# Kernel tuning notes

Measured on AMD Instinct MI355X. Metric: run time of the kernel, lower is better.

The kernel has to match this reference:

```python
import jax, jax.numpy as jnp
import numpy as np

LN_EPS = 1e-5   # torch nn.LayerNorm default
EPS = 1e-6      # module eps for denominator clamp


def _layernorm(x, gamma, beta):
    mu = jnp.mean(x, axis=-1, keepdims=True)
    var = jnp.mean(jnp.square(x - mu), axis=-1, keepdims=True)
    return (x - mu) * jax.lax.rsqrt(var + LN_EPS) * gamma + beta


def _l2norm(x):
    # torch F.normalize(dim=-1): x / max(||x||_2, 1e-12)
    n = jnp.sqrt(jnp.sum(jnp.square(x), axis=-1, keepdims=True))
    return x / jnp.maximum(n, 1e-12)


def setup_inputs() -> dict:
    key = jax.random.key(0)
    kq, kk, kv, kp = jax.random.split(key, 4)
    B, H, T, D = 4, 8, 8192, 64
    num_features = 256
    q = jax.random.normal(kq, (B, H, T, D), dtype=jnp.float32)
    k = jax.random.normal(kk, (B, H, T, D), dtype=jnp.float32)
    v = jax.random.normal(kv, (B, H, T, D), dtype=jnp.float32)
    # _create_projection with ortho=True: QR of (D, num_features) reduced -> Q is (D, D)
    g = jax.random.normal(kp, (D, num_features), dtype=jnp.float32)
    Q, _ = jnp.linalg.qr(g, mode='reduced')            # (D, D) since num_features > D
    proj = Q / jnp.maximum(jnp.sqrt(jnp.sum(Q * Q, axis=0, keepdims=True)), 1e-12)
    proj = proj * (D ** -0.25)
    gamma = jnp.ones((D,), dtype=jnp.float32)
    beta = jnp.zeros((D,), dtype=jnp.float32)
    return {"q": q, "k": k, "v": v, "proj": proj, "gamma": gamma, "beta": beta}


def reference(q, k, v, proj, gamma, beta):
    # LayerNorm over head_dim applied to q, k, v (the torch reshapes are a no-op
    # on the math: it is a per-(b,h,t) LayerNorm over the last dim D)
    qn = _layernorm(q, gamma, beta)
    kn = _layernorm(k, gamma, beta)
    vn = _layernorm(v, gamma, beta)
    qn = _l2norm(qn)
    kn = _l2norm(kn)
    # exp feature maps (clamped), scaled by 0.1
    q_proj = jnp.exp(jnp.clip(jnp.einsum('bhtn,nm->bhtm', qn, proj), -15.0, 15.0)) * 0.1
    k_proj = jnp.exp(jnp.clip(jnp.einsum('bhtn,nm->bhtm', kn, proj), -15.0, 15.0)) * 0.1
    # linear-attention accumulation
    kv = jnp.einsum('bhtm,bhtn->bhmn', k_proj, vn) * 0.1          # [B,H,M,D]
    qkv = jnp.einsum('bhtm,bhmn->bhtn', q_proj, kv) * 0.1         # [B,H,T,D]
    denom = jnp.sum(q_proj * k_proj, axis=-1, keepdims=True)      # [B,H,T,1]
    denom = jnp.maximum(denom, EPS)
    out = qkv / denom
    out = _layernorm(out, gamma, beta)                             # final LN over D
    return out  # [B,H,T,D]
```

## Files before the change

### kernel.cpp

```cpp
#include <hip/hip_runtime.h>
#include <stdint.h>
#include <stddef.h>

#define T_    8192
#define D_    64
#define BH_   32
#define CH_   32
#define ROWS_ (T_/CH_)
#define ITERS_ (ROWS_/64)
#define TS    72
#define LN_EPS 1e-5f
#define EPS_   1e-6f

#define PART_SZ   ((size_t)CH_*BH_*D_*D_*4)
#define KVF_OFF   (PART_SZ)
#define KVF_SZ    ((size_t)BH_*D_*D_*4)
#define WS_NEED   (KVF_OFF+KVF_SZ)

typedef __attribute__((ext_vector_type(8))) short bh8;
typedef __attribute__((ext_vector_type(4))) short bh4;
typedef __attribute__((ext_vector_type(4))) float f32x4;

__device__ __forceinline__ float bf2f(unsigned short u){ return __uint_as_float(((unsigned)u)<<16); }
__device__ __forceinline__ unsigned short f2bf(float f){
  unsigned u = __float_as_uint(f);
  return (unsigned short)((u + 0x7fffu + ((u>>16)&1u)) >> 16);
}
__device__ __forceinline__ void unp8(uint4 a, float* x){
  x[0]=__uint_as_float(a.x<<16); x[1]=__uint_as_float(a.x&0xffff0000u);
  x[2]=__uint_as_float(a.y<<16); x[3]=__uint_as_float(a.y&0xffff0000u);
  x[4]=__uint_as_float(a.z<<16); x[5]=__uint_as_float(a.z&0xffff0000u);
  x[6]=__uint_as_float(a.w<<16); x[7]=__uint_as_float(a.w&0xffff0000u);
}
__device__ __forceinline__ uint4 pk8(const float* x){
  uint4 r;
  r.x = (unsigned)f2bf(x[0]) | ((unsigned)f2bf(x[1])<<16);
  r.y = (unsigned)f2bf(x[2]) | ((unsigned)f2bf(x[3])<<16);
  r.z = (unsigned)f2bf(x[4]) | ((unsigned)f2bf(x[5])<<16);
  r.w = (unsigned)f2bf(x[6]) | ((unsigned)f2bf(x[7])<<16);
  return r;
}
__device__ __forceinline__ bool is_bf16_buf(const void* gamma){
  return ((const uint32_t*)gamma)[0] != 0x3F800000u;
}
__device__ __forceinline__ int vswb(int d){ return (((d&7) ^ ((d>>3)&6)) << 3); }

template<bool BF>
__device__ __forceinline__ float ldf(const void* p, long long i){
  if (BF) return bf2f(((const unsigned short*)p)[i]);
  else    return ((const float*)p)[i];
}
template<bool BF>
__device__ __forceinline__ void ld8f(const void* p, long long i, float* x){
  if (BF){ uint4 a = *(const uint4*)((const unsigned short*)p + i); unp8(a,x); }
  else {
    const float* f=(const float*)p + i;
    float4 a=*(const float4*)f, b=*(const float4*)(f+4);
    x[0]=a.x;x[1]=a.y;x[2]=a.z;x[3]=a.w; x[4]=b.x;x[5]=b.y;x[6]=b.z;x[7]=b.w;
  }
}
template<bool BF>
__device__ __forceinline__ void ld16f(const void* p, long long i, float* x){
  ld8f<BF>(p, i, x); ld8f<BF>(p, i+8, x+8);
}

__device__ __forceinline__ void ln16(float* x, const float* __restrict__ smg,
                                     const float* __restrict__ smb, int c, bool l2){
  float s=0.f;
  #pragma unroll
  for(int j=0;j<16;++j) s+=x[j];
  s += __shfl_xor(s,1); s += __shfl_xor(s,2);
  const float mu = s*(1.f/64.f);
  float vs=0.f;
  #pragma unroll
  for(int j=0;j<16;++j){ x[j]-=mu; vs=fmaf(x[j],x[j],vs); }
  vs += __shfl_xor(vs,1); vs += __shfl_xor(vs,2);
  const float rs = rsqrtf(vs*(1.f/64.f)+LN_EPS);
  float ss=0.f;
  #pragma unroll
  for(int j4=0;j4<4;++j4){
    const float4 g4 = *(const float4*)&smg[c*16+j4*4];
    const float4 b4 = *(const float4*)&smb[c*16+j4*4];
    float* xp = x + 4*j4;
    xp[0]=fmaf(xp[0]*rs, g4.x, b4.x); ss=fmaf(xp[0],xp[0],ss);
    xp[1]=fmaf(xp[1]*rs, g4.y, b4.y); ss=fmaf(xp[1],xp[1],ss);
    xp[2]=fmaf(xp[2]*rs, g4.z, b4.z); ss=fmaf(xp[2],xp[2],ss);
    xp[3]=fmaf(xp[3]*rs, g4.w, b4.w); ss=fmaf(xp[3],xp[3],ss);
  }
  if(l2){
    ss += __shfl_xor(ss,1); ss += __shfl_xor(ss,2);
    const float inv = rsqrtf(fmaxf(ss,1e-24f));
    #pragma unroll
    for(int j=0;j<16;++j) x[j]*=inv;
  }
}

template<bool BF, bool PART>
__device__ __forceinline__ void kv_body(const void* __restrict__ kg, const void* __restrict__ vg,
               const void* __restrict__ projg, const void* __restrict__ gammag,
               const void* __restrict__ betag, float* __restrict__ kvout,
               short* sm_a, short* sm_vt, short* sm_kt, float* smgb){
  const int tid=threadIdx.x, lane=tid&63, w=tid>>6;
  const int q4=lane>>4, l16=lane&15;
  const int r=lane>>2,  c=lane&3;
  const int bh=blockIdx.x;
  const long long base=(long long)bh*T_*D_;
  const int t0b=blockIdx.y*ROWS_;
  const float* smg = smgb;
  const float* smb = smgb+64;

  if (tid < 128){
    const int j = tid & 63;
    smgb[tid] = (tid<64) ? ldf<BF>(gammag,j) : ldf<BF>(betag,j);
  }
  for(int e=tid*8; e<D_*D_; e+=256*8){
    int d=e>>6, m=e&63;
    float t8[8]; ld8f<BF>(projg, e, t8);
    *(uint4*)&sm_a[d*TS+m] = pk8(t8);
  }
  __syncthreads();
  bh8 bP[4][2];
  #pragma unroll
  for(int nt=0;nt<4;++nt)
    #pragma unroll
    for(int ks=0;ks<2;++ks)
      #pragma unroll
      for(int j=0;j<8;++j)
        bP[nt][ks][j] = sm_a[(ks*32+q4*8+j)*TS + nt*16+l16];
  __syncthreads();

  f32x4 acc2[4];
  #pragma unroll
  for(int nt=0;nt<4;++nt) acc2[nt]=(f32x4){0.f,0.f,0.f,0.f};

  for(int it=0; it<ITERS_; ++it){
    const int tl=16*w;
    const long long gro = base + (long long)(t0b + it*64 + tl + r)*D_ + c*16;

    float xk[16], xv[16];
    ld16f<BF>(kg, gro, xk);
    ld16f<BF>(vg, gro, xv);

    ln16(xk, smg, smb, c, true);
    *(uint4*)&sm_a[(tl+r)*TS + c*16    ] = pk8(xk);
    *(uint4*)&sm_a[(tl+r)*TS + c*16 + 8] = pk8(xk+8);

    ln16(xv, smg, smb, c, false);
    #pragma unroll
    for(int j=0;j<16;++j){
      const int d=c*16+j;
      sm_vt[d*TS + ((tl+r) ^ vswb(d))] = (short)f2bf(xv[j]);
    }

    f32x4 c1[4];
    #pragma unroll
    for(int nt=0;nt<4;++nt) c1[nt]=(f32x4){0.f,0.f,0.f,0.f};
    #pragma unroll
    for(int ks=0;ks<2;++ks){
      bh8 af = *(const bh8*)&sm_a[(tl+l16)*TS + ks*32 + q4*8];
      #pragma unroll
      for(int nt=0;nt<4;++nt)
        c1[nt] = __builtin_amdgcn_mfma_f32_16x16x32_bf16(af, bP[nt][ks], c1[nt], 0,0,0);
    }
    #pragma unroll
    for(int nt=0;nt<4;++nt){
      bh4 p;
      #pragma unroll
      for(int reg=0;reg<4;++reg){
        float e = 0.1f*__expf(fminf(fmaxf(c1[nt][reg],-15.f),15.f));
        p[reg] = (short)f2bf(e);
      }
      *(bh4*)&sm_kt[(nt*16+l16)*TS + tl + q4*4] = p;
    }
    __syncthreads();

    #pragma unroll
    for(int ks=0;ks<2;++ks){
      bh8 af = *(const bh8*)&sm_kt[(tl+l16)*TS + ks*32 + q4*8];
      #pragma unroll
      for(int nt=0;nt<4;++nt){
        const int dn = nt*16+l16;
        bh8 bv = *(const bh8*)&sm_vt[dn*TS + ((ks*32+q4*8) ^ vswb(dn))];
        acc2[nt] = __builtin_amdgcn_mfma_f32_16x16x32_bf16(af, bv, acc2[nt], 0,0,0);
      }
    }
    __syncthreads();
  }

  if (PART){
    float* dst = kvout + ((size_t)blockIdx.y*BH_ + bh)*D_*D_;
    #pragma unroll
    for(int nt=0;nt<4;++nt)
      #pragma unroll
      for(int reg=0;reg<4;++reg)
        dst[(16*w + q4*4 + reg)*D_ + nt*16 + l16] = acc2[nt][reg]*0.1f;
  } else {
    float* dst = kvout + bh*D_*D_;
    #pragma unroll
    for(int nt=0;nt<4;++nt)
      #pragma unroll
      for(int reg=0;reg<4;++reg)
        atomicAdd(&dst[(16*w + q4*4 + reg)*D_ + nt*16 + l16], acc2[nt][reg]*0.1f);
  }
}

__global__ __launch_bounds__(256,4)
void reduce_kernel(const float* __restrict__ part, float* __restrict__ kvf){
  const int idx = blockIdx.x*256 + threadIdx.x;
  float s = 0.f;
  #pragma unroll 8
  for(int ch=0; ch<CH_; ++ch) s += part[(size_t)ch*BH_*D_*D_ + idx];
  kvf[idx] = s;
}

template<bool BF>
__device__ __forceinline__ void attn_body(const void* __restrict__ qg, const void* __restrict__ kg,
                 const void* __restrict__ projg, const void* __restrict__ gammag,
                 const void* __restrict__ betag, const float* __restrict__ kvg,
                 void* __restrict__ outg,
                 short* sm_qn, short* sm_kn, short* sm_qp, short* sm_kvT, float* smgb){
  const int tid=threadIdx.x, lane=tid&63, w=tid>>6;
  const int q4=lane>>4, l16=lane&15;
  const int r=lane>>2,  c=lane&3;
  const int bh=blockIdx.x;
  const long long base=(long long)bh*T_*D_;
  const int t0b=blockIdx.y*ROWS_;
  const float* smg = smgb;
  const float* smb = smgb+64;

  if (tid < 128){
    const int j = tid & 63;
    smgb[tid] = (tid<64) ? ldf<BF>(gammag,j) : ldf<BF>(betag,j);
  }
  for(int e=tid*8; e<D_*D_; e+=256*8){
    int d=e>>6, m=e&63;
    float t8[8]; ld8f<BF>(projg, e, t8);
    *(uint4*)&sm_qn[d*TS+m] = pk8(t8);
  }
  {
    const float* kvsrc = kvg + bh*D_*D_;
    for(int e=tid; e<D_*D_; e+=256){
      int f=e>>6, d=e&63;
      sm_kvT[d*TS + (f ^ vswb(d))] = (short)f2bf(kvsrc[e]);
    }
  }
  __syncthreads();
  bh8 bP[4][2];
  #pragma unroll
  for(int nt=0;nt<4;++nt)
    #pragma unroll
    for(int ks=0;ks<2;++ks)
      #pragma unroll
      for(int j=0;j<8;++j)
        bP[nt][ks][j] = sm_qn[(ks*32+q4*8+j)*TS + nt*16+l16];
  __syncthreads();

  for(int it=0; it<ITERS_; ++it){
    const int tl=16*w;
    const long long gro = base + (long long)(t0b + it*64 + tl + r)*D_ + c*16;

    float x[16];
    ld16f<BF>(qg, gro, x);
    ln16(x, smg, smb, c, true);
    *(uint4*)&sm_qn[(tl+r)*TS + c*16    ] = pk8(x);
    *(uint4*)&sm_qn[(tl+r)*TS + c*16 + 8] = pk8(x+8);
    ld16f<BF>(kg, gro, x);
    ln16(x, smg, smb, c, true);
    *(uint4*)&sm_kn[(tl+r)*TS + c*16    ] = pk8(x);
    *(uint4*)&sm_kn[(tl+r)*TS + c*16 + 8] = pk8(x+8);

    f32x4 qp[4], kp[4];
    #pragma unroll
    for(int nt=0;nt<4;++nt) qp[nt]=(f32x4){0.f,0.f,0.f,0.f};
    #pragma unroll
    for(int ks=0;ks<2;++ks){
      bh8 af = *(const bh8*)&sm_qn[(tl+l16)*TS + ks*32 + q4*8];
      #pragma unroll
      for(int nt=0;nt<4;++nt)
        qp[nt] = __builtin_amdgcn_mfma_f32_16x16x32_bf16(af, bP[nt][ks], qp[nt], 0,0,0);
    }
    #pragma unroll
    for(int nt=0;nt<4;++nt)
      #pragma unroll
      for(int reg=0;reg<4;++reg){
        float e = 0.1f*__expf(fminf(fmaxf(qp[nt][reg],-15.f),15.f));
        qp[nt][reg] = e;
        sm_qp[(tl+q4*4+reg)*TS + nt*16+l16] = (short)f2bf(e);
      }

    #pragma unroll
    for(int nt=0;nt<4;++nt) kp[nt]=(f32x4){0.f,0.f,0.f,0.f};
    #pragma unroll
    for(int ks=0;ks<2;++ks){
      bh8 af = *(const bh8*)&sm_kn[(tl+l16)*TS + ks*32 + q4*8];
      #pragma unroll
      for(int nt=0;nt<4;++nt)
        kp[nt] = __builtin_amdgcn_mfma_f32_16x16x32_bf16(af, bP[nt][ks], kp[nt], 0,0,0);
    }
    float sc[4];
    #pragma unroll
    for(int reg=0;reg<4;++reg){
      float dd=0.f;
      #pragma unroll
      for(int nt=0;nt<4;++nt){
        float kv = 0.1f*__expf(fminf(fmaxf(kp[nt][reg],-15.f),15.f));
        dd = fmaf(qp[nt][reg], kv, dd);
      }
      dd += __shfl_xor(dd,1); dd += __shfl_xor(dd,2);
      dd += __shfl_xor(dd,4); dd += __shfl_xor(dd,8);
      sc[reg] = 0.1f / fmaxf(dd, EPS_);
    }

    f32x4 c3[4];
    #pragma unroll
    for(int nt=0;nt<4;++nt) c3[nt]=(f32x4){0.f,0.f,0.f,0.f};
    #pragma unroll
    for(int ks=0;ks<2;++ks){
      bh8 af = *(const bh8*)&sm_qp[(tl+l16)*TS + ks*32 + q4*8];
      #pragma unroll
      for(int nt=0;nt<4;++nt){
        const int dn = nt*16+l16;
        bh8 bf = *(const bh8*)&sm_kvT[dn*TS + ((ks*32+q4*8) ^ vswb(dn))];
        c3[nt] = __builtin_amdgcn_mfma_f32_16x16x32_bf16(af, bf, c3[nt], 0,0,0);
      }
    }

    float rs4[4];
    #pragma unroll
    for(int reg=0;reg<4;++reg){
      float s=0.f;
      #pragma unroll
      for(int nt=0;nt<4;++nt){ c3[nt][reg] *= sc[reg]; s += c3[nt][reg]; }
      s += __shfl_xor(s,1); s += __shfl_xor(s,2); s += __shfl_xor(s,4); s += __shfl_xor(s,8);
      const float mu = s*(1.f/64.f);
      float vs=0.f;
      #pragma unroll
      for(int nt=0;nt<4;++nt){ const float dd=c3[nt][reg]-mu; c3[nt][reg]=dd; vs=fmaf(dd,dd,vs); }
      vs += __shfl_xor(vs,1); vs += __shfl_xor(vs,2); vs += __shfl_xor(vs,4); vs += __shfl_xor(vs,8);
      rs4[reg] = rsqrtf(vs*(1.f/64.f)+LN_EPS);
    }
    const long long obase = base + (long long)(t0b + it*64 + tl + q4*4)*D_ + l16;
    #pragma unroll
    for(int reg=0;reg<4;++reg)
      #pragma unroll
      for(int nt=0;nt<4;++nt){
        const float z = fmaf(c3[nt][reg]*rs4[reg], smg[nt*16+l16], smb[nt*16+l16]);
        const long long oi = obase + (long long)reg*D_ + nt*16;
        if (BF) ((unsigned short*)outg)[oi] = f2bf(z);
        else    ((float*)outg)[oi]          = z;
      }
  }
}

__global__ __launch_bounds__(256,4)
void kv_kernel_part(const void* __restrict__ kg, const void* __restrict__ vg,
                    const void* __restrict__ projg, const void* __restrict__ gammag,
                    const void* __restrict__ betag, float* __restrict__ part){
  __shared__ __align__(16) short sm_a [64*TS];
  __shared__ __align__(16) short sm_vt[64*TS];
  __shared__ __align__(16) short sm_kt[64*TS];
  __shared__ __align__(16) float smgb[128];
  if (is_bf16_buf(gammag)) kv_body<true ,true>(kg,vg,projg,gammag,betag,part,sm_a,sm_vt,sm_kt,smgb);
  else                     kv_body<false,true>(kg,vg,projg,gammag,betag,part,sm_a,sm_vt,sm_kt,smgb);
}

__global__ __launch_bounds__(256,4)
void kv_kernel_atomic(const void* __restrict__ kg, const void* __restrict__ vg,
                      const void* __restrict__ projg, const void* __restrict__ gammag,
                      const void* __restrict__ betag, float* __restrict__ kvg){
  __shared__ __align__(16) short sm_a [64*TS];
  __shared__ __align__(16) short sm_vt[64*TS];
  __shared__ __align__(16) short sm_kt[64*TS];
  __shared__ __align__(16) float smgb[128];
  if (is_bf16_buf(gammag)) kv_body<true ,false>(kg,vg,projg,gammag,betag,kvg,sm_a,sm_vt,sm_kt,smgb);
  else                     kv_body<false,false>(kg,vg,projg,gammag,betag,kvg,sm_a,sm_vt,sm_kt,smgb);
}

__global__ __launch_bounds__(256,4)
void attn_kernel(const void* __restrict__ qg, const void* __restrict__ kg,
                 const void* __restrict__ projg, const void* __restrict__ gammag,
                 const void* __restrict__ betag, const float* __restrict__ kvg,
                 void* __restrict__ outg){
  __shared__ __align__(16) short sm_qn [64*TS];
  __shared__ __align__(16) short sm_kn [64*TS];
  __shared__ __align__(16) short sm_qp [64*TS];
  __shared__ __align__(16) short sm_kvT[64*TS];
  __shared__ __align__(16) float smgb[128];
  if (is_bf16_buf(gammag)) attn_body<true >(qg,kg,projg,gammag,betag,kvg,outg,sm_qn,sm_kn,sm_qp,sm_kvT,smgb);
  else                     attn_body<false>(qg,kg,projg,gammag,betag,kvg,outg,sm_qn,sm_kn,sm_qp,sm_kvT,smgb);
}

extern "C" void kernel_launch(void* const* d_in, const int* in_sizes, int n_in,
                              void* d_out, int out_size, void* d_ws, size_t ws_size,
                              hipStream_t stream){
  const void* q     = d_in[0];
  const void* k     = d_in[1];
  const void* v     = d_in[2];
  const void* proj  = d_in[3];
  const void* gamma = d_in[4];
  const void* beta  = d_in[5];

  dim3 g(BH_, CH_);
  if (ws_size >= WS_NEED){
    float* part = (float*)d_ws;
    float* kvf  = (float*)((char*)d_ws + KVF_OFF);
    kv_kernel_part<<<g, 256, 0, stream>>>(k, v, proj, gamma, beta, part);
    reduce_kernel<<<dim3(BH_*D_*D_/256), 256, 0, stream>>>(part, kvf);
    attn_kernel<<<g, 256, 0, stream>>>(q, k, proj, gamma, beta, kvf, d_out);
  } else {
    float* kvf = (float*)d_ws;
    hipMemsetAsync(kvf, 0, KVF_SZ, stream);
    kv_kernel_atomic<<<g, 256, 0, stream>>>(k, v, proj, gamma, beta, kvf);
    attn_kernel<<<g, 256, 0, stream>>>(q, k, proj, gamma, beta, kvf, d_out);
  }
}
```

Before: 304.6 us.

## Prefetch next tile into registers, cache kv and gamma/beta in registers, halve chunks

Both the kv and attention kernels now load the next 64-row tile of inputs into registers while the current tile is processed, so global-load latency overlaps with compute. The attention kernel keeps the kv matrix fragments and the gamma/beta values in registers, which frees one LDS buffer. Barriers become an explicit LDS waitcnt plus s_barrier. The chunk count drops from 32 to 16 and launch bounds move from 4 to 2 blocks per SIMD, trading fewer blocks and less partial-sum reduction for higher register pressure and lower occupancy.

```diff
diff --git a/kernel.cpp b/kernel.cpp
--- a/kernel.cpp
+++ b/kernel.cpp
@@ -5,7 +5,7 @@
 #define T_    8192
 #define D_    64
 #define BH_   32
-#define CH_   32
+#define CH_   16
 #define ROWS_ (T_/CH_)
 #define ITERS_ (ROWS_/64)
 #define TS    72
@@ -44,6 +44,13 @@
   return ((const uint32_t*)gamma)[0] != 0x3F800000u;
 }
 __device__ __forceinline__ int vswb(int d){ return (((d&7) ^ ((d>>3)&6)) << 3); }
+
+__device__ __forceinline__ void block_sync_lds(){
+  __builtin_amdgcn_sched_barrier(0);
+  asm volatile("s_waitcnt lgkmcnt(0)" ::: "memory");
+  __builtin_amdgcn_s_barrier();
+  __builtin_amdgcn_sched_barrier(0);
+}
 
 template<bool BF>
 __device__ __forceinline__ float ldf(const void* p, long long i){
@@ -133,13 +140,20 @@
   #pragma unroll
   for(int nt=0;nt<4;++nt) acc2[nt]=(f32x4){0.f,0.f,0.f,0.f};
 
+  const int tl=16*w;
+  const long long grow = base + (long long)(t0b + tl + r)*D_ + c*16;
+
+  float xk[16], xv[16];
+  ld16f<BF>(kg, grow, xk);
+  ld16f<BF>(vg, grow, xv);
+
   for(int it=0; it<ITERS_; ++it){
-    const int tl=16*w;
-    const long long gro = base + (long long)(t0b + it*64 + tl + r)*D_ + c*16;
-
-    float xk[16], xv[16];
-    ld16f<BF>(kg, gro, xk);
-    ld16f<BF>(vg, gro, xv);
+    float nk[16], nv[16];
+    if (it+1 < ITERS_){
+      const long long gron = grow + (long long)(it+1)*64*D_;
+      ld16f<BF>(kg, gron, nk);
+      ld16f<BF>(vg, gron, nv);
+    }
 
     ln16(xk, smg, smb, c, true);
     *(uint4*)&sm_a[(tl+r)*TS + c*16    ] = pk8(xk);
@@ -172,7 +186,8 @@
       }
       *(bh4*)&sm_kt[(nt*16+l16)*TS + tl + q4*4] = p;
     }
-    __syncthreads();
+
+    block_sync_lds();
 
     #pragma unroll
     for(int ks=0;ks<2;++ks){
@@ -184,7 +199,13 @@
         acc2[nt] = __builtin_amdgcn_mfma_f32_16x16x32_bf16(af, bv, acc2[nt], 0,0,0);
       }
     }
-    __syncthreads();
+
+    block_sync_lds();
+
+    if (it+1 < ITERS_){
+      #pragma unroll
+      for(int j=0;j<16;++j){ xk[j]=nk[j]; xv[j]=nv[j]; }
+    }
   }
 
   if (PART){
@@ -218,7 +239,7 @@
                  const void* __restrict__ projg, const void* __restrict__ gammag,
                  const void* __restrict__ betag, const float* __restrict__ kvg,
                  void* __restrict__ outg,
-                 short* sm_qn, short* sm_kn, short* sm_qp, short* sm_kvT, float* smgb){
+                 short* sm_qn, short* sm_kn, short* sm_qp, float* smgb){
   const int tid=threadIdx.x, lane=tid&63, w=tid>>6;
   const int q4=lane>>4, l16=lane&15;
   const int r=lane>>2,  c=lane&3;
@@ -241,7 +262,7 @@
     const float* kvsrc = kvg + bh*D_*D_;
     for(int e=tid; e<D_*D_; e+=256){
       int f=e>>6, d=e&63;
-      sm_kvT[d*TS + (f ^ vswb(d))] = (short)f2bf(kvsrc[e]);
+      sm_kn[d*TS + (f ^ vswb(d))] = (short)f2bf(kvsrc[e]);
     }
   }
   __syncthreads();
@@ -253,21 +274,41 @@
       #pragma unroll
       for(int j=0;j<8;++j)
         bP[nt][ks][j] = sm_qn[(ks*32+q4*8+j)*TS + nt*16+l16];
+  bh8 bKV[4][2];
+  #pragma unroll
+  for(int nt=0;nt<4;++nt)
+    #pragma unroll
+    for(int ks=0;ks<2;++ks){
+      const int dn = nt*16+l16;
+      bKV[nt][ks] = *(const bh8*)&sm_kn[dn*TS + ((ks*32+q4*8) ^ vswb(dn))];
+    }
   __syncthreads();
 
+  float gamF[4], betF[4];
+  #pragma unroll
+  for(int nt=0;nt<4;++nt){ gamF[nt]=smg[nt*16+l16]; betF[nt]=smb[nt*16+l16]; }
+
+  const int tl=16*w;
+  const long long grow = base + (long long)(t0b + tl + r)*D_ + c*16;
+
+  float xq[16], xk[16];
+  ld16f<BF>(qg, grow, xq);
+  ld16f<BF>(kg, grow, xk);
+
   for(int it=0; it<ITERS_; ++it){
-    const int tl=16*w;
-    const long long gro = base + (long long)(t0b + it*64 + tl + r)*D_ + c*16;
-
-    float x[16];
-    ld16f<BF>(qg, gro, x);
-    ln16(x, smg, smb, c, true);
-    *(uint4*)&sm_qn[(tl+r)*TS + c*16    ] = pk8(x);
-    *(uint4*)&sm_qn[(tl+r)*TS + c*16 + 8] = pk8(x+8);
-    ld16f<BF>(kg, gro, x);
-    ln16(x, smg, smb, c, true);
-    *(uint4*)&sm_kn[(tl+r)*TS + c*16    ] = pk8(x);
-    *(uint4*)&sm_kn[(tl+r)*TS + c*16 + 8] = pk8(x+8);
+    float nq[16], nk[16];
+    if (it+1 < ITERS_){
+      const long long gron = grow + (long long)(it+1)*64*D_;
+      ld16f<BF>(qg, gron, nq);
+      ld16f<BF>(kg, gron, nk);
+    }
+
+    ln16(xq, smg, smb, c, true);
+    *(uint4*)&sm_qn[(tl+r)*TS + c*16    ] = pk8(xq);
+    *(uint4*)&sm_qn[(tl+r)*TS + c*16 + 8] = pk8(xq+8);
+    ln16(xk, smg, smb, c, true);
+    *(uint4*)&sm_kn[(tl+r)*TS + c*16    ] = pk8(xk);
+    *(uint4*)&sm_kn[(tl+r)*TS + c*16 + 8] = pk8(xk+8);
 
     f32x4 qp[4], kp[4];
     #pragma unroll
@@ -318,11 +359,8 @@
     for(int ks=0;ks<2;++ks){
       bh8 af = *(const bh8*)&sm_qp[(tl+l16)*TS + ks*32 + q4*8];
       #pragma unroll
-      for(int nt=0;nt<4;++nt){
-        const int dn = nt*16+l16;
-        bh8 bf = *(const bh8*)&sm_kvT[dn*TS + ((ks*32+q4*8) ^ vswb(dn))];
-        c3[nt] = __builtin_amdgcn_mfma_f32_16x16x32_bf16(af, bf, c3[nt], 0,0,0);
-      }
+      for(int nt=0;nt<4;++nt)
+        c3[nt] = __builtin_amdgcn_mfma_f32_16x16x32_bf16(af, bKV[nt][ks], c3[nt], 0,0,0);
     }
 
     float rs4[4];
@@ -344,15 +382,20 @@
     for(int reg=0;reg<4;++reg)
       #pragma unroll
       for(int nt=0;nt<4;++nt){
-        const float z = fmaf(c3[nt][reg]*rs4[reg], smg[nt*16+l16], smb[nt*16+l16]);
+        const float z = fmaf(c3[nt][reg]*rs4[reg], gamF[nt], betF[nt]);
         const long long oi = obase + (long long)reg*D_ + nt*16;
         if (BF) ((unsigned short*)outg)[oi] = f2bf(z);
         else    ((float*)outg)[oi]          = z;
       }
-  }
-}
-
-__global__ __launch_bounds__(256,4)
+
+    if (it+1 < ITERS_){
+      #pragma unroll
+      for(int j=0;j<16;++j){ xq[j]=nq[j]; xk[j]=nk[j]; }
+    }
+  }
+}
+
+__global__ __launch_bounds__(256,2)
 void kv_kernel_part(const void* __restrict__ kg, const void* __restrict__ vg,
                     const void* __restrict__ projg, const void* __restrict__ gammag,
                     const void* __restrict__ betag, float* __restrict__ part){
@@ -364,7 +407,7 @@
   else                     kv_body<false,true>(kg,vg,projg,gammag,betag,part,sm_a,sm_vt,sm_kt,smgb);
 }
 
-__global__ __launch_bounds__(256,4)
+__global__ __launch_bounds__(256,2)
 void kv_kernel_atomic(const void* __restrict__ kg, const void* __restrict__ vg,
                       const void* __restrict__ projg, const void* __restrict__ gammag,
                       const void* __restrict__ betag, float* __restrict__ kvg){
@@ -376,18 +419,17 @@
   else                     kv_body<false,false>(kg,vg,projg,gammag,betag,kvg,sm_a,sm_vt,sm_kt,smgb);
 }
 
-__global__ __launch_bounds__(256,4)
+__global__ __launch_bounds__(256,2)
 void attn_kernel(const void* __restrict__ qg, const void* __restrict__ kg,
                  const void* __restrict__ projg, const void* __restrict__ gammag,
                  const void* __restrict__ betag, const float* __restrict__ kvg,
                  void* __restrict__ outg){
-  __shared__ __align__(16) short sm_qn [64*TS];
-  __shared__ __align__(16) short sm_kn [64*TS];
-  __shared__ __align__(16) short sm_qp [64*TS];
-  __shared__ __align__(16) short sm_kvT[64*TS];
+  __shared__ __align__(16) short sm_qn[64*TS];
+  __shared__ __align__(16) short sm_kn[64*TS];
+  __shared__ __align__(16) short sm_qp[64*TS];
   __shared__ __align__(16) float smgb[128];
-  if (is_bf16_buf(gammag)) attn_body<true >(qg,kg,projg,gammag,betag,kvg,outg,sm_qn,sm_kn,sm_qp,sm_kvT,smgb);
-  else                     attn_body<false>(qg,kg,projg,gammag,betag,kvg,outg,sm_qn,sm_kn,sm_qp,sm_kvT,smgb);
+  if (is_bf16_buf(gammag)) attn_body<true >(qg,kg,projg,gammag,betag,kvg,outg,sm_qn,sm_kn,sm_qp,smgb);
+  else                     attn_body<false>(qg,kg,projg,gammag,betag,kvg,outg,sm_qn,sm_kn,sm_qp,smgb);
 }
 
 extern "C" void kernel_launch(void* const* d_in, const int* in_sizes, int n_in,
```

Measured after the change: 245.0 us. 1.24x faster.
